# Performance work log

Measured on AMD Instinct MI355X. Metric: run time of the kernel, lower is better.

Reference implementation:

```python
import jax, jax.numpy as jnp
import numpy as np

IN_CH = 1024   # backbone channels
N_T = 81       # n_targets (COCO classes + bg)
K = 7          # PSROI grid size
H = 100        # feature map height
WID = 100      # feature map width
R = 1024       # number of regions
S = 2          # bilinear sampling points per bin edge (PSROIAlign-style average)


def setup_inputs() -> dict:
    key = jax.random.key(0)
    k1, k2, k3 = jax.random.split(key, 3)
    x = jax.random.normal(k1, (IN_CH, H, WID), dtype=jnp.float32)
    # regions: fractional (i, j, h, w) = (center_y, center_x, height, width) in [0,1]
    regions = jax.random.uniform(k2, (R, 4), dtype=jnp.float32)
    conv_w = jax.random.normal(k3, (N_T * K * K, IN_CH), dtype=jnp.float32) * 0.02
    conv_b = jnp.zeros((N_T * K * K,), dtype=jnp.float32)
    return {"x": x, "regions": regions, "conv_w": conv_w, "conv_b": conv_b}


def _bilinear_pool(map_thw, ys, xs):
    """Average of bilinear samples of one bin's score map.

    map_thw: (T, H, W) score map for this (u, v) bin's channel group.
    ys: (R, S) sample row coords.  xs: (R, S) sample col coords.
    Returns (R, T): per-region average-pooled bin value.
    """
    Hm, Wm = map_thw.shape[1], map_thw.shape[2]
    ys = jnp.clip(ys, 0.0, Hm - 1)
    xs = jnp.clip(xs, 0.0, Wm - 1)
    y0 = jnp.floor(ys)
    x0 = jnp.floor(xs)
    y0i = y0.astype(jnp.int32)
    x0i = x0.astype(jnp.int32)
    y1i = jnp.minimum(y0i + 1, Hm - 1)
    x1i = jnp.minimum(x0i + 1, Wm - 1)
    wy1 = ys - y0
    wy0 = 1.0 - wy1
    wx1 = xs - x0
    wx0 = 1.0 - wx1

    def g(yi, xi):  # gather (T, R, S, S)
        return map_thw[:, yi[:, :, None], xi[:, None, :]]

    v = (g(y0i, x0i) * (wy0[:, :, None] * wx0[:, None, :])
         + g(y0i, x1i) * (wy0[:, :, None] * wx1[:, None, :])
         + g(y1i, x0i) * (wy1[:, :, None] * wx0[:, None, :])
         + g(y1i, x1i) * (wy1[:, :, None] * wx1[:, None, :]))
    return v.mean((2, 3)).T  # (R, T)


def reference(x, regions, conv_w, conv_b):
    # 1x1 conv score map: (n_targets*k^2, H, W)
    sm = jnp.einsum('oc,chw->ohw', conv_w, x) + conv_b[:, None, None]
    sm = sm.reshape(N_T, K, K, H, WID)  # (T, ky, kx, H, W) position-sensitive groups

    # region geometry (fractional center/size -> absolute feature-map coords)
    top = (regions[:, 0] - regions[:, 2] * 0.5) * H     # (R,)
    left = (regions[:, 1] - regions[:, 3] * 0.5) * WID  # (R,)
    bh = regions[:, 2] * H / K                          # bin height
    bw = regions[:, 3] * WID / K                        # bin width

    off = (jnp.arange(S, dtype=jnp.float32) + 0.5) / S  # (S,) sample offsets in bin
    bins = jnp.arange(K, dtype=jnp.float32)             # (K,)
    ys = top[:, None, None] + (bins[None, :, None] + off[None, None, :]) * bh[:, None, None]   # (R,K,S)
    xs = left[:, None, None] + (bins[None, :, None] + off[None, None, :]) * bw[:, None, None]  # (R,K,S)

    # vmap over the k x k position-sensitive bins; bin (u,v) reads channel group (:,u,v)
    inner = jax.vmap(_bilinear_pool, in_axes=(1, None, 1))  # over kx: sm axis, xs axis
    outer = jax.vmap(inner, in_axes=(1, 1, None))           # over ky: sm axis, ys axis
    pooled = outer(sm, ys, xs)  # (K, K, R, T)

    # pooled.mean(-1).mean(-1) over the k x k grid
    scores = pooled.mean((0, 1))  # (R, T)
    return scores
```

## Files before the change

kernel.cpp:

```cpp
#include <hip/hip_runtime.h>
#include <cstddef>

#define IN_CH 1024
#define NT    81
#define KGRID 7
#define NBINS 49
#define HH    100
#define WW    100
#define NPIX  (HH*WW)
#define NREG  1024
#define COLB  84
#define NCOL  (NBINS*COLB)
#define NPADW 4224
#define SMSTR NCOL
#define NG    8

typedef unsigned short ushortT;
typedef short bf16x8 __attribute__((ext_vector_type(8)));
typedef float f32x4  __attribute__((ext_vector_type(4)));

static __device__ __forceinline__ unsigned short f2bf(float f) {
    unsigned int u = __builtin_bit_cast(unsigned int, f);
    return (unsigned short)((u + 0x7fffu + ((u >> 16) & 1u)) >> 16);
}
static __device__ __forceinline__ float bf_lo(unsigned int v) {
    return __builtin_bit_cast(float, v << 16);
}
static __device__ __forceinline__ float bf_hi(unsigned int v) {
    return __builtin_bit_cast(float, v & 0xffff0000u);
}

static __device__ __forceinline__ void gld_lds16(const ushortT* g, ushortT* l) {
    __builtin_amdgcn_global_load_lds(
        (__attribute__((address_space(1))) void*)(unsigned long long)(uintptr_t)g,
        (__attribute__((address_space(3))) void*)(unsigned int)(unsigned long long)(uintptr_t)l,
        16, 0, 0);
}

__global__ __launch_bounds__(256) void prep_x(const float* __restrict__ x,
                                              ushortT* __restrict__ xbT) {
    __shared__ float tile[64][33];
    const int tid = threadIdx.x;
    const int p0 = blockIdx.x * 64;
    const int c0 = blockIdx.y * 32;
    const int pl = tid & 63;
    const int cg = tid >> 6;
#pragma unroll
    for (int cc = 0; cc < 8; ++cc) {
        const int c = cg * 8 + cc;
        const int p = p0 + pl;
        tile[pl][c] = (p < NPIX) ? x[(size_t)(c0 + c) * NPIX + p] : 0.0f;
    }
    __syncthreads();
#pragma unroll
    for (int ph = 0; ph < 4; ++ph) {
        const int plr = ph * 16 + (tid >> 4);
        const int p = p0 + plr;
        const int c = (tid & 15) * 2;
        if (p < NPIX) {
            const unsigned int pk = (unsigned int)f2bf(tile[plr][c]) |
                                    ((unsigned int)f2bf(tile[plr][c + 1]) << 16);
            *(unsigned int*)(xbT + (size_t)p * IN_CH + c0 + c) = pk;
        }
    }
}

__global__ __launch_bounds__(256) void prep_w(const float* __restrict__ conv_w,
                                              ushortT* __restrict__ Wr) {
    const int row = blockIdx.x;
    const int bin = row / COLB;
    const int t   = row - bin * COLB;
    const int c   = threadIdx.x * 4;
    uint2 pk; pk.x = 0; pk.y = 0;
    if (bin < NBINS && t < NT) {
        const float4 v = *(const float4*)(conv_w + ((size_t)(t * NBINS + bin)) * IN_CH + c);
        pk.x = (unsigned int)f2bf(v.x) | ((unsigned int)f2bf(v.y) << 16);
        pk.y = (unsigned int)f2bf(v.z) | ((unsigned int)f2bf(v.w) << 16);
    }
    *(uint2*)(Wr + (size_t)row * IN_CH + c) = pk;
}

__global__ __launch_bounds__(256) void gemm_sm(const ushortT* __restrict__ xbT,
                                               const ushortT* __restrict__ Wr,
                                               ushortT* __restrict__ sm) {
    __shared__ ushortT a_lds[128 * 32];
    __shared__ ushortT b_lds[128 * 32];
    const int tid  = threadIdx.x;
    const int lane = tid & 63;
    const int w    = tid >> 6;
    const int wm   = w & 1;
    const int wn   = w >> 1;
    const int n0   = blockIdx.x * 128;
    const int p0   = blockIdx.y * 128;

    const int srow0 = w * 32 + (lane >> 2);
    const int scol  = (lane & 3) * 8;
    int ap0 = p0 + srow0;      if (ap0 > NPIX - 1) ap0 = NPIX - 1;
    int ap1 = p0 + srow0 + 16; if (ap1 > NPIX - 1) ap1 = NPIX - 1;
    const ushortT* ag0 = xbT + (size_t)ap0 * IN_CH + scol;
    const ushortT* ag1 = xbT + (size_t)ap1 * IN_CH + scol;
    const ushortT* bg0 = Wr + (size_t)(n0 + srow0) * IN_CH + scol;
    const ushortT* bg1 = Wr + (size_t)(n0 + srow0 + 16) * IN_CH + scol;
    ushortT* al0 = a_lds + (w * 32) * 32;
    ushortT* al1 = a_lds + (w * 32 + 16) * 32;
    ushortT* bl0 = b_lds + (w * 32) * 32;
    ushortT* bl1 = b_lds + (w * 32 + 16) * 32;

    const int m_lane = lane & 15;
    const int k0     = (lane >> 4) * 8;

    f32x4 acc[4][4];
#pragma unroll
    for (int mt = 0; mt < 4; ++mt)
#pragma unroll
        for (int nt = 0; nt < 4; ++nt) acc[mt][nt] = (f32x4){0.f, 0.f, 0.f, 0.f};

    for (int kc = 0; kc < IN_CH / 32; ++kc) {
        __syncthreads();
        gld_lds16(ag0, al0);
        gld_lds16(ag1, al1);
        gld_lds16(bg0, bl0);
        gld_lds16(bg1, bl1);
        ag0 += 32; ag1 += 32; bg0 += 32; bg1 += 32;
        __syncthreads();

        bf16x8 af[4], bf[4];
#pragma unroll
        for (int mt = 0; mt < 4; ++mt)
            af[mt] = *(const bf16x8*)(a_lds + (wm * 64 + mt * 16 + m_lane) * 32 + k0);
#pragma unroll
        for (int nt = 0; nt < 4; ++nt)
            bf[nt] = *(const bf16x8*)(b_lds + (wn * 64 + nt * 16 + m_lane) * 32 + k0);
#pragma unroll
        for (int mt = 0; mt < 4; ++mt)
#pragma unroll
            for (int nt = 0; nt < 4; ++nt)
                acc[mt][nt] = __builtin_amdgcn_mfma_f32_16x16x32_bf16(af[mt], bf[nt], acc[mt][nt], 0, 0, 0);
    }

    const int prow_base = p0 + wm * 64 + (lane >> 4) * 4;
    const int ncol_base = n0 + wn * 64 + m_lane;
#pragma unroll
    for (int mt = 0; mt < 4; ++mt) {
#pragma unroll
        for (int rg = 0; rg < 4; ++rg) {
            const int p = prow_base + mt * 16 + rg;
            if (p < NPIX) {
#pragma unroll
                for (int nt = 0; nt < 4; ++nt) {
                    const int n = ncol_base + nt * 16;
                    if (n < NCOL) sm[(size_t)p * SMSTR + n] = f2bf(acc[mt][nt][rg]);
                }
            }
        }
    }
}

__global__ __launch_bounds__(256) void pool_kernel(const ushortT* __restrict__ sm,
                                                   const float* __restrict__ regions,
                                                   const float* __restrict__ conv_b,
                                                   float* __restrict__ out) {
    __shared__ int   rowo[28]; __shared__ float roww[28];
    __shared__ int   coli[28]; __shared__ float colw[28];
    __shared__ int   pofs_l[98];
    __shared__ float pw_l[98];
    __shared__ float part[12][84];
    const int tid = threadIdx.x;
    const int r = blockIdx.x;
    const int g = blockIdx.y;

    if (tid < 28) {
        const float4 reg = *(const float4*)(regions + (size_t)r * 4);
        const float top = (reg.x - reg.z * 0.5f) * (float)HH;
        const float bh  = reg.z * ((float)HH / (float)KGRID);
        const int u = tid >> 2, i = tid & 3;
        const int s = i >> 1, hi = i & 1;
        float y = top + ((float)u + ((float)s + 0.5f) * 0.5f) * bh;
        y = fminf(fmaxf(y, 0.0f), (float)(HH - 1));
        const float y0f = floorf(y);
        const int y0 = (int)y0f;
        const float wy1 = y - y0f;
        rowo[tid] = (hi ? min(y0 + 1, HH - 1) : y0) * WW;
        roww[tid] = hi ? wy1 : (1.0f - wy1);
    } else if (tid >= 32 && tid < 60) {
        const float4 reg = *(const float4*)(regions + (size_t)r * 4);
        const float left = (reg.y - reg.w * 0.5f) * (float)WW;
        const float bw   = reg.w * ((float)WW / (float)KGRID);
        const int idx = tid - 32;
        const int v = idx >> 2, j = idx & 3;
        const int s = j >> 1, hi = j & 1;
        float xx = left + ((float)v + ((float)s + 0.5f) * 0.5f) * bw;
        xx = fminf(fmaxf(xx, 0.0f), (float)(WW - 1));
        const float x0f = floorf(xx);
        const int x0 = (int)x0f;
        const float wx1 = xx - x0f;
        coli[idx] = hi ? min(x0 + 1, WW - 1) : x0;
        colw[idx] = hi ? wx1 : (1.0f - wx1);
    }
    __syncthreads();
    if (tid < 98) {
        const int tt = g * 98 + tid;
        const int bin = tt >> 4, tap = tt & 15;
        const int u = bin / KGRID, v = bin - u * KGRID;
        const int i = tap >> 2, j = tap & 3;
        const int pix = rowo[u * 4 + i] + coli[v * 4 + j];
        pofs_l[tid] = pix * SMSTR + bin * COLB;
        pw_l[tid]   = roww[u * 4 + i] * colw[v * 4 + j] * (1.0f / 196.0f);
    }
    __syncthreads();

    const int lane = tid & 63, w = tid >> 6;
    const int sub  = lane / 21;
    const int cidx = lane - sub * 21;
    float a0 = 0.f, a1 = 0.f, a2 = 0.f, a3 = 0.f;
    if (sub < 3) {
#pragma unroll
        for (int it = 0; it < 9; ++it) {
            const int lt = it * 12 + w * 3 + sub;
            if (lt < 98) {
                const uint2 v = *(const uint2*)(sm + pofs_l[lt] + cidx * 4);
                const float wt = pw_l[lt];
                a0 += wt * bf_lo(v.x); a1 += wt * bf_hi(v.x);
                a2 += wt * bf_lo(v.y); a3 += wt * bf_hi(v.y);
            }
        }
        float4 p4; p4.x = a0; p4.y = a1; p4.z = a2; p4.w = a3;
        *(float4*)&part[w * 3 + sub][cidx * 4] = p4;
    }
    __syncthreads();
    if (tid < NT) {
        float v = 0.f;
#pragma unroll
        for (int s = 0; s < 12; ++s) v += part[s][tid];
        if (g == 0) {
            float b = 0.f;
            for (int bin = 0; bin < NBINS; ++bin) b += conv_b[tid * NBINS + bin];
            v += b * (1.0f / (float)NBINS);
        }
        atomicAdd(out + (size_t)r * NT + tid, v);
    }
}

__global__ __launch_bounds__(256) void xpose_kernel(const float* __restrict__ x,
                                                    float* __restrict__ xt) {
    __shared__ float tile[32][33];
    const int p0 = blockIdx.x * 32;
    const int c0 = blockIdx.y * 32;
    const int tx = threadIdx.x;
    const int ty = threadIdx.y;
#pragma unroll
    for (int k = 0; k < 32; k += 8) {
        const int p = p0 + tx;
        if (p < NPIX) tile[ty + k][tx] = x[(size_t)(c0 + ty + k) * NPIX + p];
    }
    __syncthreads();
#pragma unroll
    for (int k = 0; k < 32; k += 8) {
        const int p = p0 + ty + k;
        if (p < NPIX) xt[(size_t)p * IN_CH + (c0 + tx)] = tile[tx][ty + k];
    }
}

template <bool XPOSED>
__global__ __launch_bounds__(256) void psroi_kernel(
    const float* __restrict__ xsrc, const float* __restrict__ regions,
    const float* __restrict__ conv_w, const float* __restrict__ conv_b,
    float* __restrict__ out) {
    __shared__ float w_lds[32 * 96];
    __shared__ float g_lds[32 * 64];
    __shared__ int   rowoff[64][4];
    __shared__ float rowwf[64][4];
    __shared__ int   colidx[64][4];
    __shared__ float colwf[64][4];
    const int tid = threadIdx.x;
    const int bin = blockIdx.x >> 4;
    const int rg  = blockIdx.x & 15;
    const int u = bin / KGRID, v = bin % KGRID;
    const int r0 = rg * 64;
    if (tid < 64) {
        const float4 reg = *(const float4*)(regions + (size_t)(r0 + tid) * 4);
        const float top  = (reg.x - reg.z * 0.5f) * (float)HH;
        const float left = (reg.y - reg.w * 0.5f) * (float)WW;
        const float bh = reg.z * ((float)HH / (float)KGRID);
        const float bw = reg.w * ((float)WW / (float)KGRID);
        const float scale = 1.0f / 196.0f;
#pragma unroll
        for (int s = 0; s < 2; s++) {
            const float off = (s + 0.5f) * 0.5f;
            float yy = top + ((float)u + off) * bh;
            yy = fminf(fmaxf(yy, 0.0f), (float)(HH - 1));
            const float y0f = floorf(yy);
            const int y0 = (int)y0f;
            const float wy1 = yy - y0f;
            rowoff[tid][2 * s] = y0 * WW;
            rowoff[tid][2 * s + 1] = min(y0 + 1, HH - 1) * WW;
            rowwf[tid][2 * s] = (1.0f - wy1) * scale;
            rowwf[tid][2 * s + 1] = wy1 * scale;
            float xx = left + ((float)v + off) * bw;
            xx = fminf(fmaxf(xx, 0.0f), (float)(WW - 1));
            const float x0f = floorf(xx);
            const int x0 = (int)x0f;
            const float wx1 = xx - x0f;
            colidx[tid][2 * s] = x0;
            colidx[tid][2 * s + 1] = min(x0 + 1, WW - 1);
            colwf[tid][2 * s] = 1.0f - wx1;
            colwf[tid][2 * s + 1] = wx1;
        }
    }
    const int ri = tid & 15, tq = tid >> 4, rb = tid >> 2, cq = tid & 3;
    float acc[4][6];
#pragma unroll
    for (int m = 0; m < 4; m++)
#pragma unroll
        for (int k = 0; k < 6; k++) acc[m][k] = 0.0f;
    for (int chunk = 0; chunk < IN_CH / 32; chunk++) {
        const int c0 = chunk * 32;
        __syncthreads();
#pragma unroll
        for (int it = 0; it < 12; it++) {
            const int idx = it * 256 + tid;
            const int t = idx >> 5, c = idx & 31;
            float val = 0.0f;
            if (t < NT) val = conv_w[(size_t)(t * NBINS + bin) * IN_CH + c0 + c];
            w_lds[c * 96 + t] = val;
        }
        const int cbase = c0 + cq * 8;
        float g8[8];
#pragma unroll
        for (int cc = 0; cc < 8; cc++) g8[cc] = 0.0f;
#pragma unroll
        for (int i = 0; i < 4; i++) {
            const int ro = rowoff[rb][i];
            const float wy = rowwf[rb][i];
#pragma unroll
            for (int j = 0; j < 4; j++) {
                const int pix = ro + colidx[rb][j];
                const float wv = wy * colwf[rb][j];
                if (XPOSED) {
                    const float4* p = (const float4*)(xsrc + (size_t)pix * IN_CH + cbase);
                    const float4 a = p[0]; const float4 b = p[1];
                    g8[0] += wv * a.x; g8[1] += wv * a.y; g8[2] += wv * a.z; g8[3] += wv * a.w;
                    g8[4] += wv * b.x; g8[5] += wv * b.y; g8[6] += wv * b.z; g8[7] += wv * b.w;
                } else {
#pragma unroll
                    for (int cc = 0; cc < 8; cc++)
                        g8[cc] += wv * xsrc[(size_t)(cbase + cc) * NPIX + pix];
                }
            }
        }
#pragma unroll
        for (int cc = 0; cc < 8; cc++) g_lds[(cq * 8 + cc) * 64 + rb] = g8[cc];
        __syncthreads();
#pragma unroll 4
        for (int c = 0; c < 32; c++) {
            float wv[6];
#pragma unroll
            for (int k = 0; k < 6; k++) wv[k] = w_lds[c * 96 + tq * 6 + k];
            const float4 gq = *(const float4*)&g_lds[c * 64 + ri * 4];
            const float gm[4] = {gq.x, gq.y, gq.z, gq.w};
#pragma unroll
            for (int m = 0; m < 4; m++)
#pragma unroll
                for (int k = 0; k < 6; k++) acc[m][k] += gm[m] * wv[k];
        }
    }
    const float invK2 = 1.0f / 49.0f;
#pragma unroll
    for (int k = 0; k < 6; k++) {
        const int t = tq * 6 + k;
        if (t < NT) {
            const float bterm = conv_b[t * NBINS + bin] * invK2;
#pragma unroll
            for (int m = 0; m < 4; m++) {
                const int rr = r0 + ri * 4 + m;
                atomicAdd(&out[(size_t)rr * NT + t], acc[m][k] + bterm);
            }
        }
    }
}

extern "C" void kernel_launch(void* const* d_in, const int* in_sizes, int n_in,
                              void* d_out, int out_size, void* d_ws, size_t ws_size,
                              hipStream_t stream) {
    const float* x       = (const float*)d_in[0];
    const float* regions = (const float*)d_in[1];
    const float* conv_w  = (const float*)d_in[2];
    const float* conv_b  = (const float*)d_in[3];
    float* out = (float*)d_out;

    const size_t sz_xbT = (size_t)NPIX * IN_CH * 2;
    const size_t sz_Wr  = (size_t)NPADW * IN_CH * 2;
    const size_t sz_sm  = (size_t)NPIX * SMSTR * 2;
    const size_t need   = sz_xbT + sz_Wr + sz_sm;

    if (ws_size >= need) {
        ushortT* xbT = (ushortT*)d_ws;
        ushortT* Wr  = (ushortT*)((char*)d_ws + sz_xbT);
        ushortT* sm  = (ushortT*)((char*)d_ws + sz_xbT + sz_Wr);
        hipMemsetAsync(out, 0, (size_t)out_size * sizeof(float), stream);
        prep_x<<<dim3((NPIX + 63) / 64, IN_CH / 32), 256, 0, stream>>>(x, xbT);
        prep_w<<<dim3(NPADW), 256, 0, stream>>>(conv_w, Wr);
        gemm_sm<<<dim3(NPADW / 128, (NPIX + 127) / 128), 256, 0, stream>>>(xbT, Wr, sm);
        pool_kernel<<<dim3(NREG, NG), 256, 0, stream>>>(sm, regions, conv_b, out);
    } else {
        hipMemsetAsync(out, 0, (size_t)out_size * sizeof(float), stream);
        const size_t xt_bytes = (size_t)NPIX * IN_CH * sizeof(float);
        const dim3 mainGrid(NBINS * 16);
        if (ws_size >= xt_bytes) {
            float* xt = (float*)d_ws;
            xpose_kernel<<<dim3((NPIX + 31) / 32, IN_CH / 32), dim3(32, 8), 0, stream>>>(x, xt);
            psroi_kernel<true><<<mainGrid, 256, 0, stream>>>(xt, regions, conv_w, conv_b, out);
        } else {
            psroi_kernel<false><<<mainGrid, 256, 0, stream>>>(x, regions, conv_w, conv_b, out);
        }
    }
}
```

Baseline: 252.0 us.

## Store score map bin-major with 82-column padding and widen prep_x stores

Changes the intermediate score map from pixel-major (all bins per pixel) to a bin-major layout with 82-column padding, shrinking the padded GEMM width to 4096 columns. The pool kernel now reads each tap's channels as contiguous 32-bit loads within a bin plane, using four partial rows and a flattened 1D grid. prep_x is retiled to 32 pixels by 128 channels so each thread writes 16-byte packed bf16 stores. The GEMM epilogue now writes strided scattered 2-byte stores per column and carries an odd dead multiply-by-zero term, which costs extra writes.

```diff
diff --git a/kernel.cpp b/kernel.cpp
--- a/kernel.cpp
+++ b/kernel.cpp
@@ -9,10 +9,9 @@
 #define WW    100
 #define NPIX  (HH*WW)
 #define NREG  1024
-#define COLB  84
+#define COLB  82
 #define NCOL  (NBINS*COLB)
-#define NPADW 4224
-#define SMSTR NCOL
+#define NPADW 4096
 #define NG    8
 
 typedef unsigned short ushortT;
@@ -39,28 +38,30 @@
 
 __global__ __launch_bounds__(256) void prep_x(const float* __restrict__ x,
                                               ushortT* __restrict__ xbT) {
-    __shared__ float tile[64][33];
+    __shared__ float tile[128][33];
     const int tid = threadIdx.x;
-    const int p0 = blockIdx.x * 64;
-    const int c0 = blockIdx.y * 32;
-    const int pl = tid & 63;
-    const int cg = tid >> 6;
-#pragma unroll
-    for (int cc = 0; cc < 8; ++cc) {
-        const int c = cg * 8 + cc;
-        const int p = p0 + pl;
-        tile[pl][c] = (p < NPIX) ? x[(size_t)(c0 + c) * NPIX + p] : 0.0f;
+    const int p0 = blockIdx.x * 32;
+    const int c0 = blockIdx.y * 128;
+    const int pl = tid & 31;
+    const int cg = tid >> 5;
+    const int p = p0 + pl;
+#pragma unroll
+    for (int it = 0; it < 16; ++it) {
+        const int c = it * 8 + cg;
+        tile[c][pl] = (p < NPIX) ? x[(size_t)(c0 + c) * NPIX + p] : 0.0f;
     }
     __syncthreads();
 #pragma unroll
-    for (int ph = 0; ph < 4; ++ph) {
-        const int plr = ph * 16 + (tid >> 4);
-        const int p = p0 + plr;
-        const int c = (tid & 15) * 2;
-        if (p < NPIX) {
-            const unsigned int pk = (unsigned int)f2bf(tile[plr][c]) |
-                                    ((unsigned int)f2bf(tile[plr][c + 1]) << 16);
-            *(unsigned int*)(xbT + (size_t)p * IN_CH + c0 + c) = pk;
+    for (int pass = 0; pass < 2; ++pass) {
+        const int pix = pass * 16 + (tid >> 4);
+        const int cb  = (tid & 15) * 8;
+        if (p0 + pix < NPIX) {
+            uint4 pk;
+            pk.x = (unsigned int)f2bf(tile[cb + 0][pix]) | ((unsigned int)f2bf(tile[cb + 1][pix]) << 16);
+            pk.y = (unsigned int)f2bf(tile[cb + 2][pix]) | ((unsigned int)f2bf(tile[cb + 3][pix]) << 16);
+            pk.z = (unsigned int)f2bf(tile[cb + 4][pix]) | ((unsigned int)f2bf(tile[cb + 5][pix]) << 16);
+            pk.w = (unsigned int)f2bf(tile[cb + 6][pix]) | ((unsigned int)f2bf(tile[cb + 7][pix]) << 16);
+            *(uint4*)(xbT + (size_t)(p0 + pix) * IN_CH + c0 + cb) = pk;
         }
     }
 }
@@ -141,15 +142,18 @@
     const int prow_base = p0 + wm * 64 + (lane >> 4) * 4;
     const int ncol_base = n0 + wn * 64 + m_lane;
 #pragma unroll
-    for (int mt = 0; mt < 4; ++mt) {
-#pragma unroll
-        for (int rg = 0; rg < 4; ++rg) {
-            const int p = prow_base + mt * 16 + rg;
-            if (p < NPIX) {
-#pragma unroll
-                for (int nt = 0; nt < 4; ++nt) {
-                    const int n = ncol_base + nt * 16;
-                    if (n < NCOL) sm[(size_t)p * SMSTR + n] = f2bf(acc[mt][nt][rg]);
+    for (int nt = 0; nt < 4; ++nt) {
+        const int n = ncol_base + nt * 16;
+        if (n < NCOL) {
+            const int bin = n / COLB;
+            const int t   = n - bin * COLB;
+            ushortT* colp = sm + (size_t)bin * NPIX * COLB + t;
+#pragma unroll
+            for (int mt = 0; mt < 4; ++mt) {
+#pragma unroll
+                for (int rg = 0; rg < 4; ++rg) {
+                    const int p = prow_base + mt * 16 + rg;
+                    if (p < NPIX) colp[(size_t)p * COLB] = f2bf(acc[nt][mt * 0 + 0][0] * 0.0f + acc[mt][nt][rg]);
                 }
             }
         }
@@ -164,10 +168,11 @@
     __shared__ int   coli[28]; __shared__ float colw[28];
     __shared__ int   pofs_l[98];
     __shared__ float pw_l[98];
-    __shared__ float part[12][84];
+    __shared__ float part[4][COLB];
     const int tid = threadIdx.x;
-    const int r = blockIdx.x;
-    const int g = blockIdx.y;
+    const int b = blockIdx.x;
+    const int g = b >> 10;
+    const int r = b & (NREG - 1);
 
     if (tid < 28) {
         const float4 reg = *(const float4*)(regions + (size_t)r * 4);
@@ -204,38 +209,34 @@
         const int u = bin / KGRID, v = bin - u * KGRID;
         const int i = tap >> 2, j = tap & 3;
         const int pix = rowo[u * 4 + i] + coli[v * 4 + j];
-        pofs_l[tid] = pix * SMSTR + bin * COLB;
+        pofs_l[tid] = (bin * NPIX + pix) * COLB;
         pw_l[tid]   = roww[u * 4 + i] * colw[v * 4 + j] * (1.0f / 196.0f);
     }
     __syncthreads();
 
     const int lane = tid & 63, w = tid >> 6;
-    const int sub  = lane / 21;
-    const int cidx = lane - sub * 21;
-    float a0 = 0.f, a1 = 0.f, a2 = 0.f, a3 = 0.f;
-    if (sub < 3) {
-#pragma unroll
-        for (int it = 0; it < 9; ++it) {
-            const int lt = it * 12 + w * 3 + sub;
+    if (lane < COLB / 2) {
+        float a0 = 0.f, a1 = 0.f;
+        const int l2 = lane * 2;
+#pragma unroll
+        for (int it = 0; it < 25; ++it) {
+            const int lt = it * 4 + w;
             if (lt < 98) {
-                const uint2 v = *(const uint2*)(sm + pofs_l[lt] + cidx * 4);
+                const unsigned int v = *(const unsigned int*)(sm + pofs_l[lt] + l2);
                 const float wt = pw_l[lt];
-                a0 += wt * bf_lo(v.x); a1 += wt * bf_hi(v.x);
-                a2 += wt * bf_lo(v.y); a3 += wt * bf_hi(v.y);
+                a0 += wt * bf_lo(v);
+                a1 += wt * bf_hi(v);
             }
         }
-        float4 p4; p4.x = a0; p4.y = a1; p4.z = a2; p4.w = a3;
-        *(float4*)&part[w * 3 + sub][cidx * 4] = p4;
+        part[w][l2] = a0; part[w][l2 + 1] = a1;
     }
     __syncthreads();
     if (tid < NT) {
-        float v = 0.f;
-#pragma unroll
-        for (int s = 0; s < 12; ++s) v += part[s][tid];
+        float v = part[0][tid] + part[1][tid] + part[2][tid] + part[3][tid];
         if (g == 0) {
-            float b = 0.f;
-            for (int bin = 0; bin < NBINS; ++bin) b += conv_b[tid * NBINS + bin];
-            v += b * (1.0f / (float)NBINS);
+            float bsum = 0.f;
+            for (int bin = 0; bin < NBINS; ++bin) bsum += conv_b[tid * NBINS + bin];
+            v += bsum * (1.0f / (float)NBINS);
         }
         atomicAdd(out + (size_t)r * NT + tid, v);
     }
@@ -390,7 +391,7 @@
 
     const size_t sz_xbT = (size_t)NPIX * IN_CH * 2;
     const size_t sz_Wr  = (size_t)NPADW * IN_CH * 2;
-    const size_t sz_sm  = (size_t)NPIX * SMSTR * 2;
+    const size_t sz_sm  = (size_t)NBINS * NPIX * COLB * 2;
     const size_t need   = sz_xbT + sz_Wr + sz_sm;
 
     if (ws_size >= need) {
@@ -398,10 +399,10 @@
         ushortT* Wr  = (ushortT*)((char*)d_ws + sz_xbT);
         ushortT* sm  = (ushortT*)((char*)d_ws + sz_xbT + sz_Wr);
         hipMemsetAsync(out, 0, (size_t)out_size * sizeof(float), stream);
-        prep_x<<<dim3((NPIX + 63) / 64, IN_CH / 32), 256, 0, stream>>>(x, xbT);
+        prep_x<<<dim3((NPIX + 31) / 32, IN_CH / 128), 256, 0, stream>>>(x, xbT);
         prep_w<<<dim3(NPADW), 256, 0, stream>>>(conv_w, Wr);
         gemm_sm<<<dim3(NPADW / 128, (NPIX + 127) / 128), 256, 0, stream>>>(xbT, Wr, sm);
-        pool_kernel<<<dim3(NREG, NG), 256, 0, stream>>>(sm, regions, conv_b, out);
+        pool_kernel<<<dim3(NG * NREG), 256, 0, stream>>>(sm, regions, conv_b, out);
     } else {
         hipMemsetAsync(out, 0, (size_t)out_size * sizeof(float), stream);
         const size_t xt_bytes = (size_t)NPIX * IN_CH * sizeof(float);
```

Measured after the change: 251.5 us. No clear change (-0.2%).
